# Performance work log

Measured on AMD Instinct MI355X. Metric: run time of the kernel, lower is better.

## Reference

```python
import jax, jax.numpy as jnp
import numpy as np

TOPK = 300
NUM_LEVELS = 3
GATE_TEMP = 1.0


def _normalized_grid(h, w):
    # matches torch: linspace(-1,1) meshgrid 'ij', stack (xx, yy) -> [h*w, 2]
    y = jnp.linspace(-1.0, 1.0, h, dtype=jnp.float32)
    x = jnp.linspace(-1.0, 1.0, w, dtype=jnp.float32)
    yy, xx = jnp.meshgrid(y, x, indexing='ij')
    return jnp.stack((xx, yy), axis=-1).reshape(h * w, 2)


def setup_inputs() -> dict:
    key = jax.random.key(0)
    ks = jax.random.split(key, 10)
    C, H_DIM, MAXL = 256, 256, 8
    shapes = [(8, C, 100, 152), (8, C, 50, 76), (8, C, 25, 38)]
    inp = {}
    for i, s in enumerate(shapes):
        inp[f'f{i}'] = jax.random.normal(ks[i], s, dtype=jnp.float32)
    inp['conv_w'] = jax.random.normal(ks[3], (C,), dtype=jnp.float32) * (1.0 / np.sqrt(C))
    inp['conv_b'] = jnp.zeros((1,), dtype=jnp.float32)
    inp['level_emb'] = jax.random.normal(ks[4], (MAXL, H_DIM), dtype=jnp.float32)
    qin = C + H_DIM + 3  # 515
    inp['w1'] = jax.random.normal(ks[5], (qin, H_DIM), dtype=jnp.float32) * (1.0 / np.sqrt(qin))
    inp['b1'] = jnp.zeros((H_DIM,), dtype=jnp.float32)
    inp['w2'] = jax.random.normal(ks[6], (H_DIM, H_DIM), dtype=jnp.float32) * (1.0 / np.sqrt(H_DIM))
    inp['b2'] = jnp.zeros((H_DIM,), dtype=jnp.float32)
    inp['gate_w'] = jax.random.normal(ks[7], (H_DIM, MAXL), dtype=jnp.float32) * (1.0 / np.sqrt(H_DIM))
    inp['gate_b'] = jnp.zeros((MAXL,), dtype=jnp.float32)
    inp['residual_scale'] = jnp.zeros((1,), dtype=jnp.float32)  # residual_scale_init=0.0
    return inp


def reference(f0, f1, f2, conv_w, conv_b, level_emb, w1, b1, w2, b2, gate_w, gate_b, residual_scale):
    levels = [f0, f1, f2]
    B = f0.shape[0]
    tok_s, tok_f, tok_p, tok_l = [], [], [], []
    for i, f in enumerate(levels):
        _, C, H, W = f.shape
        # 1x1 conv proxy objectness score -> [B, H*W]
        s = jnp.einsum('bchw,c->bhw', f, conv_w).reshape(B, H * W) + conv_b[0]
        tok_s.append(s)
        tok_f.append(f.reshape(B, C, H * W).transpose(0, 2, 1))       # [B, HW, C]
        tok_p.append(jnp.broadcast_to(_normalized_grid(H, W), (B, H * W, 2)))
        tok_l.append(jnp.full((B, H * W), i, dtype=jnp.int32))
    scores = jnp.concatenate(tok_s, axis=1)   # [B, N]
    feats = jnp.concatenate(tok_f, axis=1)    # [B, N, C]
    pos = jnp.concatenate(tok_p, axis=1)      # [B, N, 2]
    lvl = jnp.concatenate(tok_l, axis=1)      # [B, N]

    top_vals, top_idx = jax.lax.top_k(scores, TOPK)                     # [B, K]
    fk = jnp.take_along_axis(feats, top_idx[:, :, None], axis=1)        # [B, K, C]
    pk = jnp.take_along_axis(pos, top_idx[:, :, None], axis=1)          # [B, K, 2]
    lk = jnp.take_along_axis(lvl, top_idx, axis=1)                      # [B, K]
    sp = jax.nn.sigmoid(top_vals)                                       # [B, K]

    q = jnp.concatenate([fk, level_emb[lk], pk, sp[..., None]], axis=-1)  # [B, K, C+H+3]
    h = jax.nn.relu(q @ w1 + b1)
    h = jax.nn.relu(h @ w2 + b2)
    logits = (h @ gate_w + gate_b)[..., :NUM_LEVELS]                     # [B, K, L]
    gates = jax.nn.softmax(logits / GATE_TEMP, axis=-1)
    alpha = gates.mean(axis=1)                                           # [B, L]
    scale = 1.0 + residual_scale[0] * alpha                              # [B, L]

    outs = [f * scale[:, i][:, None, None, None] for i, f in enumerate(levels)]
    # flatten the output feature dict into one [B, sum(C*H*W)] array
    return jnp.concatenate([o.reshape(B, -1) for o in outs], axis=1)
```

## Files before the change

### kernel.cpp

```cpp
#include <hip/hip_runtime.h>
#include <hip/hip_bf16.h>

#define NTOK 19950
#define NTOK2 9975
#define KTOP 300
#define NB 8
#define NQ (NB * KTOP)
#define QDIM 520

typedef float f32x4 __attribute__((ext_vector_type(4)));

__device__ __forceinline__ uint32_t fkey(float f) {
    uint32_t u = __float_as_uint(f);
    return (u & 0x80000000u) ? ~u : (u | 0x80000000u);
}

__global__ __launch_bounds__(256) void score_kernel(
    const float* __restrict__ f0, const float* __restrict__ f1, const float* __restrict__ f2,
    const float* __restrict__ conv_w, const float* __restrict__ conv_b,
    float* __restrict__ scores)
{
    __shared__ float cw[256];
    cw[threadIdx.x] = conv_w[threadIdx.x];
    __syncthreads();
    int t = blockIdx.x * 256 + threadIdx.x;
    if (t >= NB * NTOK2) return;
    int b = t / NTOK2;
    int pos = (t - b * NTOK2) * 2;
    const float* f; int HWl, hw;
    if (pos < 15200)      { f = f0; HWl = 15200; hw = pos; }
    else if (pos < 19000) { f = f1; HWl = 3800;  hw = pos - 15200; }
    else                  { f = f2; HWl = 950;   hw = pos - 19000; }
    const float2* base = (const float2*)(f + (size_t)b * 256 * HWl + hw);
    const int stride2 = HWl >> 1;
    float s0 = 0.0f, s1 = 0.0f;
    #pragma unroll 16
    for (int c = 0; c < 256; ++c) {
        float2 v = base[(size_t)c * stride2];
        s0 += v.x * cw[c];
        s1 += v.y * cw[c];
    }
    scores[b * NTOK + pos]     = s0 + conv_b[0];
    scores[b * NTOK + pos + 1] = s1 + conv_b[0];
}

__global__ __launch_bounds__(1024, 1) void topk_kernel(
    const float* __restrict__ scores, int* __restrict__ top_idx)
{
    __shared__ uint32_t key[NTOK];
    __shared__ int whist[16][256];
    __shared__ int suffix[256];
    __shared__ uint32_t s_prefix;
    __shared__ int s_Kr, s_cnt, s_tcnt;
    __shared__ int tie[1024];
    const int tid = threadIdx.x;
    const int wv = tid >> 6;
    const int b = blockIdx.x;
    const float* srow = scores + b * NTOK;
    for (int i = tid; i < NTOK; i += 1024) key[i] = fkey(srow[i]);
    if (tid == 0) { s_prefix = 0u; s_Kr = KTOP; }
    __syncthreads();
    uint32_t pmask = 0u;
    for (int pass = 0; pass < 4; ++pass) {
        const int shift = 24 - 8 * pass;
        for (int i = tid; i < 16 * 256; i += 1024) ((int*)whist)[i] = 0;
        __syncthreads();
        const uint32_t prefix = s_prefix;
        const int Kr = s_Kr;
        for (int i = tid; i < NTOK; i += 1024) {
            uint32_t k = key[i];
            if ((k & pmask) == prefix) atomicAdd(&whist[wv][(k >> shift) & 255], 1);
        }
        __syncthreads();
        if (tid < 256) {
            int s = 0;
            #pragma unroll
            for (int w = 0; w < 16; ++w) s += whist[w][tid];
            suffix[tid] = s;
        }
        __syncthreads();
        for (int off = 1; off < 256; off <<= 1) {
            int t = 0;
            if (tid < 256 && tid + off < 256) t = suffix[tid + off];
            __syncthreads();
            if (tid < 256) suffix[tid] += t;
            __syncthreads();
        }
        if (tid < 256) {
            int sgeq = suffix[tid];
            int sgt  = (tid < 255) ? suffix[tid + 1] : 0;
            if (sgeq >= Kr && sgt < Kr) {
                s_prefix = prefix | ((uint32_t)tid << shift);
                s_Kr = Kr - sgt;
            }
        }
        __syncthreads();
        pmask |= (0xFFu << shift);
    }
    const uint32_t T = s_prefix;
    const int need = s_Kr;
    if (tid == 0) { s_cnt = 0; s_tcnt = 0; }
    __syncthreads();
    for (int i = tid; i < NTOK; i += 1024) {
        uint32_t k = key[i];
        if (k > T) {
            int p = atomicAdd(&s_cnt, 1);
            top_idx[b * KTOP + p] = i;
        } else if (k == T) {
            int p = atomicAdd(&s_tcnt, 1);
            if (p < 1024) tie[p] = i;
        }
    }
    __syncthreads();
    if (tid == 0) {
        int base = s_cnt;
        int tcnt = s_tcnt > 1024 ? 1024 : s_tcnt;
        for (int s = 0; s < need; ++s) {
            int mi = s;
            for (int u = s + 1; u < tcnt; ++u) if (tie[u] < tie[mi]) mi = u;
            int tmp = tie[s]; tie[s] = tie[mi]; tie[mi] = tmp;
            top_idx[b * KTOP + base + s] = tie[s];
        }
    }
}

__global__ __launch_bounds__(256) void gather_kernel(
    const float* __restrict__ f0, const float* __restrict__ f1, const float* __restrict__ f2,
    const float* __restrict__ scores, const int* __restrict__ top_idx,
    const float* __restrict__ level_emb, float* __restrict__ Q)
{
    const int k = blockIdx.x;
    const int b = k / KTOP;
    const int idx = top_idx[k];
    int lvl, hw, HWl, Wl, Hl;
    if (idx < 15200)      { lvl = 0; hw = idx;         HWl = 15200; Wl = 152; Hl = 100; }
    else if (idx < 19000) { lvl = 1; hw = idx - 15200; HWl = 3800;  Wl = 76;  Hl = 50;  }
    else                  { lvl = 2; hw = idx - 19000; HWl = 950;   Wl = 38;  Hl = 25;  }
    const float* f = (lvl == 0) ? f0 : ((lvl == 1) ? f1 : f2);
    const int c = threadIdx.x;
    float* qr = Q + (size_t)k * QDIM;
    qr[c]       = f[((size_t)b * 256 + c) * HWl + hw];
    qr[256 + c] = level_emb[lvl * 256 + c];
    if (c < 8) {
        float v = 0.0f;
        if (c == 0) {
            int hh = hw / Wl, ww = hw - hh * Wl;
            v = -1.0f + 2.0f * (float)ww / (float)(Wl - 1);
        } else if (c == 1) {
            int hh = hw / Wl;
            v = -1.0f + 2.0f * (float)hh / (float)(Hl - 1);
        } else if (c == 2) {
            float sv = scores[b * NTOK + idx];
            v = 1.0f / (1.0f + expf(-sv));
        }
        qr[512 + c] = v;
    }
}

#define QT 8
__global__ __launch_bounds__(512, 1) void mlp_kernel(
    const float* __restrict__ Q,
    const float* __restrict__ w1, const float* __restrict__ b1,
    const float* __restrict__ w2, const float* __restrict__ b2,
    const float* __restrict__ gate_w, const float* __restrict__ gate_b,
    float* __restrict__ G)
{
    __shared__ __align__(16) float q[QT][QDIM];
    __shared__ __align__(16) float part[QT][256];
    __shared__ __align__(16) float h[QT][256];
    const int tid = threadIdx.x;
    const int out = tid & 255;
    const int kh = tid >> 8;
    const int k0 = blockIdx.x * QT;

    {
        const float4* Qg = (const float4*)(Q + (size_t)k0 * QDIM);
        float4* qs = (float4*)&q[0][0];
        for (int i = tid; i < QT * QDIM / 4; i += 512) qs[i] = Qg[i];
    }
    __syncthreads();

    float acc[QT];

    {
        #pragma unroll
        for (int t = 0; t < QT; ++t) acc[t] = 0.0f;
        const float* wp = w1 + (size_t)(kh * 256) * 256 + out;
        float a0 = wp[0], a1 = wp[256], a2 = wp[512], a3 = wp[768];
        for (int i4 = 0; i4 < 64; ++i4) {
            float c0 = a0, c1 = a1, c2 = a2, c3 = a3;
            const float* wn = wp + 1024;
            if (i4 < 63) { a0 = wn[0]; a1 = wn[256]; a2 = wn[512]; a3 = wn[768]; }
            wp = wn;
            const int kb = kh * 256 + i4 * 4;
            #pragma unroll
            for (int t = 0; t < QT; ++t) {
                float4 qv = *reinterpret_cast<const float4*>(&q[t][kb]);
                acc[t] += qv.x * c0 + qv.y * c1 + qv.z * c2 + qv.w * c3;
            }
        }
        if (kh) {
            for (int r = 512; r < 515; ++r) {
                float wv = w1[(size_t)r * 256 + out];
                #pragma unroll
                for (int t = 0; t < QT; ++t) acc[t] += q[t][r] * wv;
            }
            #pragma unroll
            for (int t = 0; t < QT; ++t) part[t][out] = acc[t];
        }
    }
    __syncthreads();
    if (kh == 0) {
        float bj = b1[out];
        #pragma unroll
        for (int t = 0; t < QT; ++t) h[t][out] = fmaxf(acc[t] + part[t][out] + bj, 0.0f);
    }
    __syncthreads();

    {
        #pragma unroll
        for (int t = 0; t < QT; ++t) acc[t] = 0.0f;
        const float* wp = w2 + (size_t)(kh * 128) * 256 + out;
        float a0 = wp[0], a1 = wp[256], a2 = wp[512], a3 = wp[768];
        for (int i4 = 0; i4 < 32; ++i4) {
            float c0 = a0, c1 = a1, c2 = a2, c3 = a3;
            const float* wn = wp + 1024;
            if (i4 < 31) { a0 = wn[0]; a1 = wn[256]; a2 = wn[512]; a3 = wn[768]; }
            wp = wn;
            const int kb = kh * 128 + i4 * 4;
            #pragma unroll
            for (int t = 0; t < QT; ++t) {
                float4 hv = *reinterpret_cast<const float4*>(&h[t][kb]);
                acc[t] += hv.x * c0 + hv.y * c1 + hv.z * c2 + hv.w * c3;
            }
        }
        if (kh) {
            #pragma unroll
            for (int t = 0; t < QT; ++t) part[t][out] = acc[t];
        }
    }
    __syncthreads();
    if (kh == 0) {
        float bj = b2[out];
        #pragma unroll
        for (int t = 0; t < QT; ++t) q[t][out] = fmaxf(acc[t] + part[t][out] + bj, 0.0f);
    }
    __syncthreads();

    if (tid < 256) {
        const int t = tid >> 5, seg = tid & 31;
        float l0 = 0.f, l1 = 0.f, l2 = 0.f;
        for (int c = seg * 8; c < seg * 8 + 8; ++c) {
            float hv = q[t][c];
            l0 += hv * gate_w[c * 8 + 0];
            l1 += hv * gate_w[c * 8 + 1];
            l2 += hv * gate_w[c * 8 + 2];
        }
        float* gp = &part[0][0];
        gp[(t * 32 + seg) * 3 + 0] = l0;
        gp[(t * 32 + seg) * 3 + 1] = l1;
        gp[(t * 32 + seg) * 3 + 2] = l2;
    }
    __syncthreads();
    if (tid < QT) {
        const int t = tid;
        float l0 = gate_b[0], l1 = gate_b[1], l2 = gate_b[2];
        const float* gp = &part[0][0];
        for (int seg = 0; seg < 32; ++seg) {
            l0 += gp[(t * 32 + seg) * 3 + 0];
            l1 += gp[(t * 32 + seg) * 3 + 1];
            l2 += gp[(t * 32 + seg) * 3 + 2];
        }
        float m = fmaxf(l0, fmaxf(l1, l2));
        float e0 = expf(l0 - m), e1 = expf(l1 - m), e2 = expf(l2 - m);
        float inv = 1.0f / (e0 + e1 + e2);
        G[(k0 + t) * 3 + 0] = e0 * inv;
        G[(k0 + t) * 3 + 1] = e1 * inv;
        G[(k0 + t) * 3 + 2] = e2 * inv;
    }
}

__global__ __launch_bounds__(256) void out_kernel(
    const f32x4* __restrict__ f0, const f32x4* __restrict__ f1, const f32x4* __restrict__ f2,
    const float* __restrict__ G, const float* __restrict__ rs, f32x4* __restrict__ out)
{
    __shared__ float red[3][32];
    __shared__ float ssc[3];
    const int b = blockIdx.y;
    const int tid = threadIdx.x;
    if (tid < 96) {
        const int l = tid / 32, c = tid % 32;
        float s = 0.0f;
        const int kb = c * 10;
        const int ke = (kb + 10 < KTOP) ? kb + 10 : KTOP;
        for (int k = kb; k < ke; ++k) s += G[(size_t)(b * KTOP + k) * 3 + l];
        red[l][c] = s;
    }
    __syncthreads();
    for (int off = 16; off > 0; off >>= 1) {
        if (tid < 96) {
            const int l = tid / 32, c = tid % 32;
            if (c < off) red[l][c] += red[l][c + off];
        }
        __syncthreads();
    }
    if (tid < 3) ssc[tid] = 1.0f + rs[0] * (red[tid][0] / (float)KTOP);
    __syncthreads();

    const int t0 = blockIdx.x * 256 + tid;
    const int TPB = gridDim.x * 256;
    f32x4* ob = out + (size_t)b * 1276800;
    {
        const float sc = ssc[0];
        const f32x4* src = f0 + (size_t)b * 972800;
        for (int r = t0; r < 972800; r += TPB)
            __builtin_nontemporal_store(src[r] * sc, &ob[r]);
    }
    {
        const float sc = ssc[1];
        const f32x4* src = f1 + (size_t)b * 243200;
        f32x4* o1 = ob + 972800;
        for (int r = t0; r < 243200; r += TPB)
            __builtin_nontemporal_store(src[r] * sc, &o1[r]);
    }
    {
        const float sc = ssc[2];
        const f32x4* src = f2 + (size_t)b * 60800;
        f32x4* o2 = ob + 1216000;
        for (int r = t0; r < 60800; r += TPB)
            __builtin_nontemporal_store(src[r] * sc, &o2[r]);
    }
}

extern "C" void kernel_launch(void* const* d_in, const int* in_sizes, int n_in,
                              void* d_out, int out_size, void* d_ws, size_t ws_size,
                              hipStream_t stream)
{
    const float* f0        = (const float*)d_in[0];
    const float* f1        = (const float*)d_in[1];
    const float* f2        = (const float*)d_in[2];
    const float* conv_w    = (const float*)d_in[3];
    const float* conv_b    = (const float*)d_in[4];
    const float* level_emb = (const float*)d_in[5];
    const float* w1        = (const float*)d_in[6];
    const float* b1        = (const float*)d_in[7];
    const float* w2        = (const float*)d_in[8];
    const float* b2        = (const float*)d_in[9];
    const float* gate_w    = (const float*)d_in[10];
    const float* gate_b    = (const float*)d_in[11];
    const float* rs        = (const float*)d_in[12];

    char* ws = (char*)d_ws;
    float* scores   = (float*)ws;
    int*   top_idx  = (int*)(ws + 640 * 1024);
    float* G        = (float*)(ws + 656 * 1024);
    float* Q        = (float*)(ws + 704 * 1024);

    score_kernel<<<(NB * NTOK2 + 255) / 256, 256, 0, stream>>>(
        f0, f1, f2, conv_w, conv_b, scores);
    topk_kernel<<<NB, 1024, 0, stream>>>(scores, top_idx);
    gather_kernel<<<NQ, 256, 0, stream>>>(f0, f1, f2, scores, top_idx, level_emb, Q);
    mlp_kernel<<<NQ / QT, 512, 0, stream>>>(Q, w1, b1, w2, b2, gate_w, gate_b, G);
    out_kernel<<<dim3(256, NB), 256, 0, stream>>>((const f32x4*)f0, (const f32x4*)f1,
                                                  (const f32x4*)f2, G, rs, (f32x4*)d_out);
}
```

Before: 159.3 us.

## Fuse gather into MLP, widen score loads, use wave-shuffle suffix scan

The gather kernel is removed and its work moves into the MLP kernel, which now reads the selected feature columns, level embeddings, positions and sigmoid scores straight into shared memory. This drops one launch and the round trip through the Q workspace buffer. The score kernel now uses float4 loads per thread for levels 0 and 1 (float2 for level 2), and the top-k suffix scan uses one wave of shuffles in place of a barrier-heavy log-step loop. The gathered feature loads inside the MLP kernel are strided and uncoalesced, so they may stall that kernel before its compute starts.

```diff
diff --git a/kernel.cpp b/kernel.cpp
--- a/kernel.cpp
+++ b/kernel.cpp
@@ -2,11 +2,11 @@
 #include <hip/hip_bf16.h>
 
 #define NTOK 19950
-#define NTOK2 9975
 #define KTOP 300
 #define NB 8
 #define NQ (NB * KTOP)
 #define QDIM 520
+#define SCW 5225
 
 typedef float f32x4 __attribute__((ext_vector_type(4)));
 
@@ -24,24 +24,46 @@
     cw[threadIdx.x] = conv_w[threadIdx.x];
     __syncthreads();
     int t = blockIdx.x * 256 + threadIdx.x;
-    if (t >= NB * NTOK2) return;
-    int b = t / NTOK2;
-    int pos = (t - b * NTOK2) * 2;
-    const float* f; int HWl, hw;
-    if (pos < 15200)      { f = f0; HWl = 15200; hw = pos; }
-    else if (pos < 19000) { f = f1; HWl = 3800;  hw = pos - 15200; }
-    else                  { f = f2; HWl = 950;   hw = pos - 19000; }
-    const float2* base = (const float2*)(f + (size_t)b * 256 * HWl + hw);
-    const int stride2 = HWl >> 1;
-    float s0 = 0.0f, s1 = 0.0f;
-    #pragma unroll 16
-    for (int c = 0; c < 256; ++c) {
-        float2 v = base[(size_t)c * stride2];
-        s0 += v.x * cw[c];
-        s1 += v.y * cw[c];
-    }
-    scores[b * NTOK + pos]     = s0 + conv_b[0];
-    scores[b * NTOK + pos + 1] = s1 + conv_b[0];
+    if (t >= NB * SCW) return;
+    const int b = t / SCW;
+    const int r = t - b * SCW;
+    const float cb = conv_b[0];
+    if (r < 3800) {
+        const float* base = f0 + (size_t)b * 256 * 15200 + r * 4;
+        float s0 = 0.f, s1 = 0.f, s2 = 0.f, s3 = 0.f;
+        #pragma unroll 16
+        for (int c = 0; c < 256; ++c) {
+            float4 v = *reinterpret_cast<const float4*>(base + (size_t)c * 15200);
+            float w = cw[c];
+            s0 += v.x * w; s1 += v.y * w; s2 += v.z * w; s3 += v.w * w;
+        }
+        float* so = scores + b * NTOK + r * 4;
+        so[0] = s0 + cb; so[1] = s1 + cb; so[2] = s2 + cb; so[3] = s3 + cb;
+    } else if (r < 4750) {
+        const int r1 = r - 3800;
+        const float* base = f1 + (size_t)b * 256 * 3800 + r1 * 4;
+        float s0 = 0.f, s1 = 0.f, s2 = 0.f, s3 = 0.f;
+        #pragma unroll 16
+        for (int c = 0; c < 256; ++c) {
+            float4 v = *reinterpret_cast<const float4*>(base + (size_t)c * 3800);
+            float w = cw[c];
+            s0 += v.x * w; s1 += v.y * w; s2 += v.z * w; s3 += v.w * w;
+        }
+        float* so = scores + b * NTOK + 15200 + r1 * 4;
+        so[0] = s0 + cb; so[1] = s1 + cb; so[2] = s2 + cb; so[3] = s3 + cb;
+    } else {
+        const int r2 = r - 4750;
+        const float* base = f2 + (size_t)b * 256 * 950 + r2 * 2;
+        float s0 = 0.f, s1 = 0.f;
+        #pragma unroll 16
+        for (int c = 0; c < 256; ++c) {
+            float2 v = *reinterpret_cast<const float2*>(base + (size_t)c * 950);
+            float w = cw[c];
+            s0 += v.x * w; s1 += v.y * w;
+        }
+        float* so = scores + b * NTOK + 19000 + r2 * 2;
+        so[0] = s0 + cb; so[1] = s1 + cb;
+    }
 }
 
 __global__ __launch_bounds__(1024, 1) void topk_kernel(
@@ -49,7 +71,7 @@
 {
     __shared__ uint32_t key[NTOK];
     __shared__ int whist[16][256];
-    __shared__ int suffix[256];
+    __shared__ int suffix[257];
     __shared__ uint32_t s_prefix;
     __shared__ int s_Kr, s_cnt, s_tcnt;
     __shared__ int tie[1024];
@@ -58,7 +80,7 @@
     const int b = blockIdx.x;
     const float* srow = scores + b * NTOK;
     for (int i = tid; i < NTOK; i += 1024) key[i] = fkey(srow[i]);
-    if (tid == 0) { s_prefix = 0u; s_Kr = KTOP; }
+    if (tid == 0) { s_prefix = 0u; s_Kr = KTOP; suffix[256] = 0; }
     __syncthreads();
     uint32_t pmask = 0u;
     for (int pass = 0; pass < 4; ++pass) {
@@ -79,16 +101,26 @@
             suffix[tid] = s;
         }
         __syncthreads();
-        for (int off = 1; off < 256; off <<= 1) {
-            int t = 0;
-            if (tid < 256 && tid + off < 256) t = suffix[tid + off];
-            __syncthreads();
-            if (tid < 256) suffix[tid] += t;
-            __syncthreads();
-        }
+        if (tid < 64) {
+            const int c0 = suffix[tid * 4], c1 = suffix[tid * 4 + 1];
+            const int c2 = suffix[tid * 4 + 2], c3 = suffix[tid * 4 + 3];
+            const int tot = c0 + c1 + c2 + c3;
+            int s = tot;
+            #pragma unroll
+            for (int off = 1; off < 64; off <<= 1) {
+                int o = __shfl_down(s, off);
+                if (tid + off < 64) s += o;
+            }
+            const int Sn = s - tot;
+            suffix[tid * 4 + 3] = c3 + Sn;
+            suffix[tid * 4 + 2] = c2 + c3 + Sn;
+            suffix[tid * 4 + 1] = c1 + c2 + c3 + Sn;
+            suffix[tid * 4 + 0] = tot + Sn;
+        }
+        __syncthreads();
         if (tid < 256) {
             int sgeq = suffix[tid];
-            int sgt  = (tid < 255) ? suffix[tid + 1] : 0;
+            int sgt  = suffix[tid + 1];
             if (sgeq >= Kr && sgt < Kr) {
                 s_prefix = prefix | ((uint32_t)tid << shift);
                 s_Kr = Kr - sgt;
@@ -124,42 +156,11 @@
     }
 }
 
-__global__ __launch_bounds__(256) void gather_kernel(
+#define QT 8
+__global__ __launch_bounds__(512, 1) void mlp_kernel(
     const float* __restrict__ f0, const float* __restrict__ f1, const float* __restrict__ f2,
     const float* __restrict__ scores, const int* __restrict__ top_idx,
-    const float* __restrict__ level_emb, float* __restrict__ Q)
-{
-    const int k = blockIdx.x;
-    const int b = k / KTOP;
-    const int idx = top_idx[k];
-    int lvl, hw, HWl, Wl, Hl;
-    if (idx < 15200)      { lvl = 0; hw = idx;         HWl = 15200; Wl = 152; Hl = 100; }
-    else if (idx < 19000) { lvl = 1; hw = idx - 15200; HWl = 3800;  Wl = 76;  Hl = 50;  }
-    else                  { lvl = 2; hw = idx - 19000; HWl = 950;   Wl = 38;  Hl = 25;  }
-    const float* f = (lvl == 0) ? f0 : ((lvl == 1) ? f1 : f2);
-    const int c = threadIdx.x;
-    float* qr = Q + (size_t)k * QDIM;
-    qr[c]       = f[((size_t)b * 256 + c) * HWl + hw];
-    qr[256 + c] = level_emb[lvl * 256 + c];
-    if (c < 8) {
-        float v = 0.0f;
-        if (c == 0) {
-            int hh = hw / Wl, ww = hw - hh * Wl;
-            v = -1.0f + 2.0f * (float)ww / (float)(Wl - 1);
-        } else if (c == 1) {
-            int hh = hw / Wl;
-            v = -1.0f + 2.0f * (float)hh / (float)(Hl - 1);
-        } else if (c == 2) {
-            float sv = scores[b * NTOK + idx];
-            v = 1.0f / (1.0f + expf(-sv));
-        }
-        qr[512 + c] = v;
-    }
-}
-
-#define QT 8
-__global__ __launch_bounds__(512, 1) void mlp_kernel(
-    const float* __restrict__ Q,
+    const float* __restrict__ level_emb,
     const float* __restrict__ w1, const float* __restrict__ b1,
     const float* __restrict__ w2, const float* __restrict__ b2,
     const float* __restrict__ gate_w, const float* __restrict__ gate_b,
@@ -168,15 +169,38 @@
     __shared__ __align__(16) float q[QT][QDIM];
     __shared__ __align__(16) float part[QT][256];
     __shared__ __align__(16) float h[QT][256];
+    __shared__ int s_b[QT], s_lvl[QT], s_hw[QT], s_HW[QT];
     const int tid = threadIdx.x;
     const int out = tid & 255;
     const int kh = tid >> 8;
     const int k0 = blockIdx.x * QT;
 
-    {
-        const float4* Qg = (const float4*)(Q + (size_t)k0 * QDIM);
-        float4* qs = (float4*)&q[0][0];
-        for (int i = tid; i < QT * QDIM / 4; i += 512) qs[i] = Qg[i];
+    if (tid < QT) {
+        const int kk = k0 + tid;
+        const int bq = kk / KTOP;
+        const int idx = top_idx[kk];
+        int lvl, hw, HWl, Wl, Hl;
+        if (idx < 15200)      { lvl = 0; hw = idx;         HWl = 15200; Wl = 152; Hl = 100; }
+        else if (idx < 19000) { lvl = 1; hw = idx - 15200; HWl = 3800;  Wl = 76;  Hl = 50;  }
+        else                  { lvl = 2; hw = idx - 19000; HWl = 950;   Wl = 38;  Hl = 25;  }
+        s_b[tid] = bq; s_lvl[tid] = lvl; s_hw[tid] = hw; s_HW[tid] = HWl;
+        int hh = hw / Wl, ww = hw - hh * Wl;
+        float x = -1.0f + 2.0f * (float)ww / (float)(Wl - 1);
+        float y = -1.0f + 2.0f * (float)hh / (float)(Hl - 1);
+        float sv = scores[bq * NTOK + idx];
+        float sp = 1.0f / (1.0f + expf(-sv));
+        q[tid][512] = x; q[tid][513] = y; q[tid][514] = sp;
+        q[tid][515] = 0.0f; q[tid][516] = 0.0f; q[tid][517] = 0.0f;
+        q[tid][518] = 0.0f; q[tid][519] = 0.0f;
+    }
+    __syncthreads();
+    #pragma unroll
+    for (int j = tid; j < QT * 256; j += 512) {
+        const int t = j >> 8, c = j & 255;
+        const int lvl = s_lvl[t];
+        const float* f = (lvl == 0) ? f0 : ((lvl == 1) ? f1 : f2);
+        q[t][c]       = f[((size_t)(s_b[t] * 256 + c)) * s_HW[t] + s_hw[t]];
+        q[t][256 + c] = level_emb[lvl * 256 + c];
     }
     __syncthreads();
 
@@ -354,13 +378,12 @@
     float* scores   = (float*)ws;
     int*   top_idx  = (int*)(ws + 640 * 1024);
     float* G        = (float*)(ws + 656 * 1024);
-    float* Q        = (float*)(ws + 704 * 1024);
-
-    score_kernel<<<(NB * NTOK2 + 255) / 256, 256, 0, stream>>>(
+
+    score_kernel<<<(NB * SCW + 255) / 256, 256, 0, stream>>>(
         f0, f1, f2, conv_w, conv_b, scores);
     topk_kernel<<<NB, 1024, 0, stream>>>(scores, top_idx);
-    gather_kernel<<<NQ, 256, 0, stream>>>(f0, f1, f2, scores, top_idx, level_emb, Q);
-    mlp_kernel<<<NQ / QT, 512, 0, stream>>>(Q, w1, b1, w2, b2, gate_w, gate_b, G);
+    mlp_kernel<<<NQ / QT, 512, 0, stream>>>(f0, f1, f2, scores, top_idx, level_emb,
+                                            w1, b1, w2, b2, gate_w, gate_b, G);
     out_kernel<<<dim3(256, NB), 256, 0, stream>>>((const f32x4*)f0, (const f32x4*)f1,
                                                   (const f32x4*)f2, G, rs, (f32x4*)d_out);
 }
```

After: 161.8 us. No clear change (+1.5%).
